# Kernel tuning notes

Measured on AMD Instinct MI355X. Metric: run time of the kernel, lower is better.

Reference implementation:

```python
import jax, jax.numpy as jnp
import numpy as np

N_GENE, N_TRAIN, N_EDGES = 20000, 4096, 131072
SRC, DST, H, OUT, NC = 2500, 2675, 2500, 2500, 16
EPS = 1e-5
SLOPE = 0.01  # torch default leaky_relu negative slope


def _leaky(x):
    return jnp.where(x >= 0, x, SLOPE * x)


def _bn(x, g, b):
    # BatchNorm1d, training-mode batch statistics over the node (batch) dim
    m = x.mean(axis=0)
    v = x.var(axis=0)
    return (x - m) * jax.lax.rsqrt(v + EPS) * g + b


def _ln(x, g, b):
    m = x.mean(axis=-1, keepdims=True)
    v = x.var(axis=-1, keepdims=True)
    return (x - m) * jax.lax.rsqrt(v + EPS) * g + b


def _sage(src_f, dst_f, si, di, W_self, W_neigh, b, n_dst):
    # DGL SAGEConv 'mean': fc_self(h_dst) + fc_neigh(mean over in-neighbors)
    msg = src_f[si]                                            # [E, d_src] gather
    agg = jax.ops.segment_sum(msg, di, num_segments=n_dst)     # [n_dst, d_src]
    deg = jax.ops.segment_sum(jnp.ones((si.shape[0],), src_f.dtype), di, num_segments=n_dst)
    mean = agg / jnp.maximum(deg, 1.0)[:, None]
    return dst_f @ W_self + mean @ W_neigh + b


def setup_inputs() -> dict:
    key = jax.random.key(0)
    ks = jax.random.split(key, 20)
    s = 0.02  # weight scale to keep deep 2500-dim chain numerically tame
    n = lambda k, shp: jax.random.normal(k, shp, dtype=jnp.float32)
    return {
        'gene_feats': n(ks[0], (N_GENE, SRC)),
        'train_feats': n(ks[1], (N_TRAIN, DST - NC)),
        'y_hat': n(ks[2], (N_TRAIN, NC)),
        'edge_src': jax.random.randint(ks[3], (N_EDGES,), 0, N_GENE, dtype=jnp.int32),
        'edge_dst': jax.random.randint(ks[4], (N_EDGES,), 0, N_TRAIN, dtype=jnp.int32),
        'W_self3': n(ks[5], (DST, H)) * s, 'W_neigh3': n(ks[6], (SRC, H)) * s, 'b3': jnp.zeros((H,), jnp.float32),
        'bn3_g': jnp.ones((H,), jnp.float32), 'bn3_b': jnp.zeros((H,), jnp.float32),
        'Wq': n(ks[7], (H, H)) * s, 'Wk': n(ks[8], (H, H)) * s, 'Wv': n(ks[9], (H, H)) * s,
        'bq': jnp.zeros((H,), jnp.float32), 'bk': jnp.zeros((H,), jnp.float32), 'bv': jnp.zeros((H,), jnp.float32),
        'Wo': n(ks[10], (H, H)) * s, 'bo': jnp.zeros((H,), jnp.float32),
        'ln2_g': jnp.ones((H,), jnp.float32), 'ln2_b': jnp.zeros((H,), jnp.float32),
        'W_self4': n(ks[11], (H, OUT)) * s, 'W_neigh4': n(ks[12], (SRC, OUT)) * s, 'b4': jnp.zeros((OUT,), jnp.float32),
        'bn4_g': jnp.ones((OUT,), jnp.float32), 'bn4_b': jnp.zeros((OUT,), jnp.float32),
        'W_lin2': n(ks[13], (OUT, OUT)) * s, 'b_lin2': jnp.zeros((OUT,), jnp.float32),
        'W_ce': n(ks[14], (OUT, NC)) * s, 'b_ce': jnp.zeros((NC,), jnp.float32),
    }


def reference(gene_feats, train_feats, y_hat, edge_src, edge_dst,
              W_self3, W_neigh3, b3, bn3_g, bn3_b,
              Wq, Wk, Wv, bq, bk, bv, Wo, bo, ln2_g, ln2_b,
              W_self4, W_neigh4, b4, bn4_g, bn4_b,
              W_lin2, b_lin2, W_ce, b_ce):
    # concat label logits onto train-node features (dst dim -> 2675)
    dst = jnp.concatenate([train_feats, y_hat], axis=1)
    # conv3: bipartite SAGE gene_node -> train_node
    h = _sage(gene_feats, dst, edge_src, edge_dst, W_self3, W_neigh3, b3, N_TRAIN)
    h = _leaky(_bn(h, bn3_g, bn3_b))
    # single-head self-attention over ALL train nodes as one sequence [L=N_TRAIN, E=H]
    q = h @ Wq + bq
    k = h @ Wk + bk
    v = h @ Wv + bv
    attn = jax.nn.softmax(q @ k.T * (1.0 / jnp.sqrt(jnp.asarray(H, h.dtype))), axis=-1)
    h = (attn @ v) @ Wo + bo
    h = _leaky(_ln(h, ln2_g, ln2_b))
    # (dropout omitted: eval-mode identity)
    # conv4: same graph, src = raw gene feats, dst = attention output
    h = _sage(gene_feats, h, edge_src, edge_dst, W_self4, W_neigh4, b4, N_TRAIN)
    x_hat = _leaky(_bn(h, bn4_g, bn4_b))
    y = jax.nn.relu(x_hat @ W_lin2 + b_lin2) @ W_ce + b_ce
    return (x_hat, y)
```

## Files before the change

kernel.cpp:

```cpp
#include <hip/hip_runtime.h>
#include <hip/hip_bf16.h>
#include <cstdint>
#include <cstddef>

constexpr int NTRAIN = 4096;
constexpr int NEDGES = 131072;
constexpr int DSRC = 2500, DH = 2500, DNC = 16;
constexpr int KD1 = 2659;
constexpr int KC3 = 5175;
constexpr int KP3 = 5184;
constexpr int KC4 = 5000;
constexpr int KP4 = 5056;
constexpr int KPH = 2560;
constexpr int NPW = 2560;
constexpr int GSTR = 2504;
constexpr float EPSV = 1e-5f;
constexpr float SLOPEV = 0.01f;

typedef __attribute__((ext_vector_type(8))) short bf16x8;
typedef __attribute__((ext_vector_type(4))) float f32x4;

static __device__ __forceinline__ unsigned short bfbits(float f) {
    __hip_bfloat16 h = __float2bfloat16(f);
    return *reinterpret_cast<unsigned short*>(&h);
}
static __device__ __forceinline__ float b2f(short s) {
    return __uint_as_float(((unsigned)(unsigned short)s) << 16);
}

__global__ void count_deg_k(const int* __restrict__ edst, int* __restrict__ deg) {
    int e = blockIdx.x * 256 + threadIdx.x;
    if (e < NEDGES) atomicAdd(&deg[edst[e]], 1);
}

__global__ __launch_bounds__(1024) void scan_deg_k(const int* __restrict__ deg,
                                                   int* __restrict__ indptr,
                                                   int* __restrict__ cursor) {
    __shared__ int sums[1024];
    int t = threadIdx.x;
    int base = t * 4;
    int d0 = deg[base + 0], d1 = deg[base + 1], d2 = deg[base + 2], d3 = deg[base + 3];
    sums[t] = d0 + d1 + d2 + d3;
    __syncthreads();
    for (int o = 1; o < 1024; o <<= 1) {
        int v = (t >= o) ? sums[t - o] : 0;
        __syncthreads();
        sums[t] += v;
        __syncthreads();
    }
    int excl = (t == 0) ? 0 : sums[t - 1];
    int p0 = excl, p1 = p0 + d0, p2 = p1 + d1, p3 = p2 + d2;
    indptr[base + 0] = p0; indptr[base + 1] = p1; indptr[base + 2] = p2; indptr[base + 3] = p3;
    cursor[base + 0] = p0; cursor[base + 1] = p1; cursor[base + 2] = p2; cursor[base + 3] = p3;
    if (t == 1023) indptr[4096] = p3 + d3;
}

__global__ void scatter_edges_k(const int* __restrict__ esrc, const int* __restrict__ edst,
                                int* __restrict__ cursor, int* __restrict__ csr_src) {
    int e = blockIdx.x * 256 + threadIdx.x;
    if (e < NEDGES) {
        int d = edst[e];
        int p = atomicAdd(&cursor[d], 1);
        csr_src[p] = esrc[e];
    }
}

__global__ __launch_bounds__(256) void gene2bf_k(const float* __restrict__ gene,
                                                 short* __restrict__ gbf) {
    int v = blockIdx.x * 256 + threadIdx.x;
    if (v >= 313) return;
    int row = blockIdx.y;
    const float* src = gene + (size_t)row * DSRC + v * 8;
    f32x4 a = *(const f32x4*)(src);
    f32x4 b = {0.f, 0.f, 0.f, 0.f};
    if (v < 312) b = *(const f32x4*)(src + 4);
    bf16x8 o;
#pragma unroll
    for (int c = 0; c < 4; c++) o[c] = (short)bfbits(a[c]);
#pragma unroll
    for (int c = 0; c < 4; c++) o[4 + c] = (short)bfbits(b[c]);
    *(bf16x8*)(gbf + (size_t)row * GSTR + v * 8) = o;
}

__global__ __launch_bounds__(256) void sage_mean_k(const short* __restrict__ gbf,
                                                   const int* __restrict__ indptr,
                                                   const int* __restrict__ csr_src,
                                                   __hip_bfloat16* __restrict__ A3,
                                                   __hip_bfloat16* __restrict__ A4) {
    int row = blockIdx.x;
    int s = indptr[row], e = indptr[row + 1];
    int t = threadIdx.x;
    float a0[8], a1[8];
#pragma unroll
    for (int c = 0; c < 8; c++) { a0[c] = 0.f; a1[c] = 0.f; }
    bool has1 = (t < 57);
    int j = s;
    for (; j + 2 <= e; j += 2) {
        const bf16x8* g0 = (const bf16x8*)(gbf + (size_t)csr_src[j] * GSTR);
        const bf16x8* g1 = (const bf16x8*)(gbf + (size_t)csr_src[j + 1] * GSTR);
        bf16x8 u0 = g0[t], w0 = g1[t];
        bf16x8 u1, w1;
        if (has1) { u1 = g0[t + 256]; w1 = g1[t + 256]; }
#pragma unroll
        for (int c = 0; c < 8; c++) a0[c] += b2f(u0[c]) + b2f(w0[c]);
        if (has1) {
#pragma unroll
            for (int c = 0; c < 8; c++) a1[c] += b2f(u1[c]) + b2f(w1[c]);
        }
    }
    if (j < e) {
        const bf16x8* g0 = (const bf16x8*)(gbf + (size_t)csr_src[j] * GSTR);
        bf16x8 u0 = g0[t];
#pragma unroll
        for (int c = 0; c < 8; c++) a0[c] += b2f(u0[c]);
        if (has1) {
            bf16x8 u1 = g0[t + 256];
#pragma unroll
            for (int c = 0; c < 8; c++) a1[c] += b2f(u1[c]);
        }
    }
    float inv = 1.f / fmaxf((float)(e - s), 1.f);
#pragma unroll
    for (int c = 0; c < 8; c++) {
        int f = t * 8 + c;
        __hip_bfloat16 h = __float2bfloat16(a0[c] * inv);
        A3[(size_t)row * KP3 + 2675 + f] = h;
        A4[(size_t)row * KP4 + 2500 + f] = h;
    }
    if (has1) {
#pragma unroll
        for (int c = 0; c < 8; c++) {
            int f = (t + 256) * 8 + c;
            if (f < 2500) {
                __hip_bfloat16 h = __float2bfloat16(a1[c] * inv);
                A3[(size_t)row * KP3 + 2675 + f] = h;
                A4[(size_t)row * KP4 + 2500 + f] = h;
            }
        }
    }
}

__global__ void dst_build_k(const float* __restrict__ trainf, const float* __restrict__ yhat,
                            __hip_bfloat16* __restrict__ A3) {
    int c = blockIdx.x * 256 + threadIdx.x;
    int r = blockIdx.y;
    if (c >= KP3) return;
    if (c >= 2675 && c < KC3) return;
    float v = 0.f;
    if (c < KD1) v = trainf[(size_t)r * KD1 + c];
    else if (c < 2675) v = yhat[r * DNC + (c - KD1)];
    A3[(size_t)r * KP3 + c] = __float2bfloat16(v);
}

__global__ __launch_bounds__(256) void wtrans_k(const float* __restrict__ W1,
                                                const float* __restrict__ W2, int ldw,
                                                __hip_bfloat16* __restrict__ Wt,
                                                int Nreal, int K1, int K12, int Kpad, int Npad) {
    __shared__ float tile[32][33];
    int k0 = blockIdx.x * 32, n0 = blockIdx.y * 32;
    int x = threadIdx.x & 31, y = threadIdx.x >> 5;
#pragma unroll
    for (int i = 0; i < 32; i += 8) {
        int k = k0 + y + i, n = n0 + x;
        float v = 0.f;
        if (n < Nreal) {
            if (k < K1) v = W1[(size_t)k * ldw + n];
            else if (k < K12) v = W2[(size_t)(k - K1) * ldw + n];
        }
        tile[y + i][x] = v;
    }
    __syncthreads();
#pragma unroll
    for (int i = 0; i < 32; i += 8) {
        int n = n0 + y + i, k = k0 + x;
        if (n < Npad && k < Kpad) Wt[(size_t)n * Kpad + k] = __float2bfloat16(tile[x][y + i]);
    }
}

__device__ __forceinline__ void async_cp16(const void* g, void* l) {
    __builtin_amdgcn_global_load_lds((const __attribute__((address_space(1))) void*)g,
                                     (__attribute__((address_space(3))) void*)l, 16, 0, 0);
}
#define WAITVM(N) asm volatile("s_waitcnt vmcnt(" #N ")" ::: "memory")
static __device__ __forceinline__ void bar_raw() {
    asm volatile("" ::: "memory");
    __builtin_amdgcn_s_barrier();
    asm volatile("" ::: "memory");
}

__global__ __launch_bounds__(512, 2) void gemm256_k(const short* __restrict__ A,
                                                    const short* __restrict__ Bt,
                                                    const float* __restrict__ bias,
                                                    float* __restrict__ Cf,
                                                    __hip_bfloat16* __restrict__ Cb,
                                                    int N, int K, int sA, int sB, int ldc,
                                                    float alpha, int act) {
    __shared__ short smem[65536];
    int nwg = gridDim.x * gridDim.y;
    int orig = blockIdx.y * gridDim.x + blockIdx.x;
    int qd = nwg >> 3, rr = nwg & 7;
    int xcd = orig & 7, oidx = orig >> 3;
    int nb = (xcd < rr ? xcd * (qd + 1) : rr * (qd + 1) + (xcd - rr) * qd) + oidx;
    int bx = nb % gridDim.x, by = nb / gridDim.x;
    int row0 = by * 256, col0 = bx * 256;

    int tid = threadIdx.x;
    int wave = tid >> 6, lane = tid & 63;
    int wm = wave >> 2, wn = wave & 3;

    int rsub = lane >> 2;
    int cs = ((lane & 3) * 8) ^ ((lane >= 32) ? 16 : 0);
    const short* gA0 = A + (size_t)(row0 + wave * 16 + rsub) * sA + cs;
    const short* gA1 = A + (size_t)(row0 + wave * 16 + 128 + rsub) * sA + cs;
    const short* gB0 = Bt + (size_t)(col0 + wave * 16 + rsub) * sB + cs;
    const short* gB1 = Bt + (size_t)(col0 + wave * 16 + 128 + rsub) * sB + cs;
    int sa0 = wave * 1024;
    int sa1 = (wave + 8) * 1024;

    int fr = lane & 15, kq = lane >> 4;
    int roff = fr * 32 + ((kq * 8) ^ ((fr & 8) ? 16 : 0));

    f32x4 acc[8][4];
#pragma unroll
    for (int i = 0; i < 8; i++)
#pragma unroll
        for (int j = 0; j < 4; j++)
#pragma unroll
            for (int r = 0; r < 4; r++) acc[i][j][r] = 0.f;

#define STAGE_A(kb, b, k0s) { \
    short* l0 = smem + (b) * 32768 + sa0 + (kb) * 512; \
    short* l1 = smem + (b) * 32768 + sa1 + (kb) * 512; \
    async_cp16(gA0 + (k0s) + (kb) * 32, l0); \
    async_cp16(gA1 + (k0s) + (kb) * 32, l1); }
#define STAGE_B(kb, b, k0s) { \
    short* l0 = smem + (b) * 32768 + 16384 + sa0 + (kb) * 512; \
    short* l1 = smem + (b) * 32768 + 16384 + sa1 + (kb) * 512; \
    async_cp16(gB0 + (k0s) + (kb) * 32, l0); \
    async_cp16(gB1 + (k0s) + (kb) * 32, l1); }
#define PHASE(b, kk, mq) { \
    const short* ab = smem + (b) * 32768; \
    const short* bb = smem + (b) * 32768 + 16384; \
    bf16x8 af[4], bv[4]; \
    _Pragma("unroll") for (int i = 0; i < 4; i++) \
        af[i] = *(const bf16x8*)(ab + (((wm * 8 + (mq) * 4 + i) * 2 + (kk)) << 9) + roff); \
    _Pragma("unroll") for (int j = 0; j < 4; j++) \
        bv[j] = *(const bf16x8*)(bb + (((wn * 4 + j) * 2 + (kk)) << 9) + roff); \
    __builtin_amdgcn_s_setprio(1); \
    _Pragma("unroll") for (int i = 0; i < 4; i++) \
        _Pragma("unroll") for (int j = 0; j < 4; j++) \
            acc[(mq) * 4 + i][j] = __builtin_amdgcn_mfma_f32_16x16x32_bf16(af[i], bv[j], acc[(mq) * 4 + i][j], 0, 0, 0); \
    __builtin_amdgcn_s_setprio(0); }

    int nt = K >> 6;
    STAGE_A(0, 0, 0); STAGE_B(0, 0, 0); STAGE_A(1, 0, 0); STAGE_B(1, 0, 0);
    int buf = 0;
    for (int t = 0; t < nt - 1; ++t) {
        int k1 = (t + 1) << 6;
        WAITVM(4); bar_raw();
        STAGE_A(0, buf ^ 1, k1);
        PHASE(buf, 0, 0);
        STAGE_B(0, buf ^ 1, k1);
        PHASE(buf, 0, 1);
        WAITVM(4); bar_raw();
        STAGE_A(1, buf ^ 1, k1);
        PHASE(buf, 1, 0);
        STAGE_B(1, buf ^ 1, k1);
        PHASE(buf, 1, 1);
        buf ^= 1;
    }
    WAITVM(4); bar_raw();
    PHASE(buf, 0, 0); PHASE(buf, 0, 1);
    WAITVM(0); bar_raw();
    PHASE(buf, 1, 0); PHASE(buf, 1, 1);
#undef STAGE_A
#undef STAGE_B
#undef PHASE

    int cn = lane & 15, cm = kq * 4;
    int mbase = row0 + wm * 128, nbase = col0 + wn * 64;
    if (Cb) {
#pragma unroll
        for (int j = 0; j < 4; j++) {
            int n = nbase + j * 16 + cn;
            if (n >= ldc) continue;
            bool real = n < N;
            float bvv = (real && bias) ? bias[n] : 0.f;
#pragma unroll
            for (int i = 0; i < 8; i++) {
#pragma unroll
                for (int r = 0; r < 4; r++) {
                    int m = mbase + i * 16 + cm + r;
                    float c = real ? alpha * acc[i][j][r] + bvv : 0.f;
                    if (act) c = fmaxf(c, 0.f);
                    Cb[(size_t)m * ldc + n] = __float2bfloat16(c);
                }
            }
        }
    } else {
#pragma unroll
        for (int j = 0; j < 4; j++) {
            int n = nbase + j * 16 + cn;
            if (n >= N) continue;
            float bvv = bias ? bias[n] : 0.f;
#pragma unroll
            for (int i = 0; i < 8; i++) {
#pragma unroll
                for (int r = 0; r < 4; r++) {
                    int m = mbase + i * 16 + cm + r;
                    float c = alpha * acc[i][j][r] + bvv;
                    if (act) c = fmaxf(c, 0.f);
                    Cf[(size_t)m * ldc + n] = c;
                }
            }
        }
    }
}

__global__ __launch_bounds__(256) void bn_partial_k(const float* __restrict__ X,
                                                    double* __restrict__ ps, double* __restrict__ ps2,
                                                    int M, int Ncol, int rowsPer) {
    int c = blockIdx.x * 256 + threadIdx.x;
    if (c >= Ncol) return;
    int r0 = blockIdx.y * rowsPer;
    int r1 = min(r0 + rowsPer, M);
    double s = 0, s2 = 0;
    for (int r = r0; r < r1; r++) {
        float x = X[(size_t)r * Ncol + c];
        s += x;
        s2 += (double)x * x;
    }
    ps[(size_t)blockIdx.y * Ncol + c] = s;
    ps2[(size_t)blockIdx.y * Ncol + c] = s2;
}

__global__ void bn_finalize_k(const double* __restrict__ ps, const double* __restrict__ ps2,
                              const float* __restrict__ g, const float* __restrict__ b,
                              float* __restrict__ scale, float* __restrict__ shift,
                              int Ncol, int nParts, int M) {
    int c = blockIdx.x * 256 + threadIdx.x;
    if (c >= Ncol) return;
    double s = 0, s2 = 0;
    for (int p = 0; p < nParts; p++) {
        s += ps[(size_t)p * Ncol + c];
        s2 += ps2[(size_t)p * Ncol + c];
    }
    double m = s / M;
    double v = s2 / M - m * m;
    float sc = g[c] / sqrtf((float)v + EPSV);
    scale[c] = sc;
    shift[c] = b[c] - (float)m * sc;
}

__global__ void bn_apply_k(const float* __restrict__ X, const float* __restrict__ scale,
                           const float* __restrict__ shift, __hip_bfloat16* __restrict__ Yb,
                           float* __restrict__ Yf, int Nreal, int Cpad) {
    int c = blockIdx.x * 256 + threadIdx.x;
    int r = blockIdx.y;
    if (c >= Cpad) return;
    float v = 0.f;
    if (c < Nreal) {
        v = fmaf(X[(size_t)r * Nreal + c], scale[c], shift[c]);
        v = v >= 0.f ? v : SLOPEV * v;
        if (Yf) Yf[(size_t)r * Nreal + c] = v;
    }
    Yb[(size_t)r * Cpad + c] = __float2bfloat16(v);
}

__device__ __forceinline__ double wave_sum_d(double v) {
#pragma unroll
    for (int o = 32; o > 0; o >>= 1) v += __shfl_down(v, o, 64);
    return v;
}
__device__ __forceinline__ float wave_sum_f(float v) {
#pragma unroll
    for (int o = 32; o > 0; o >>= 1) v += __shfl_down(v, o, 64);
    return v;
}
__device__ __forceinline__ float wave_max_f(float v) {
#pragma unroll
    for (int o = 32; o > 0; o >>= 1) v = fmaxf(v, __shfl_down(v, o, 64));
    return v;
}

__global__ __launch_bounds__(256) void ln_leaky_k(const float* __restrict__ X,
                                                  const float* __restrict__ g,
                                                  const float* __restrict__ b,
                                                  __hip_bfloat16* __restrict__ A4) {
    int row = blockIdx.x;
    const float* xr = X + (size_t)row * DH;
    double s = 0, s2 = 0;
    for (int c = threadIdx.x; c < DH; c += 256) {
        float x = xr[c];
        s += x;
        s2 += (double)x * x;
    }
    __shared__ double sb[4], sb2[4];
    int lane = threadIdx.x & 63, w = threadIdx.x >> 6;
    s = wave_sum_d(s);
    s2 = wave_sum_d(s2);
    if (lane == 0) { sb[w] = s; sb2[w] = s2; }
    __syncthreads();
    double S = sb[0] + sb[1] + sb[2] + sb[3];
    double S2 = sb2[0] + sb2[1] + sb2[2] + sb2[3];
    double m = S / DH;
    double v = S2 / DH - m * m;
    float inv = 1.f / sqrtf((float)v + EPSV);
    float mf = (float)m;
    __hip_bfloat16* yr = A4 + (size_t)row * KP4;
    for (int c = threadIdx.x; c < DH; c += 256) {
        float x = (xr[c] - mf) * inv * g[c] + b[c];
        x = x >= 0.f ? x : SLOPEV * x;
        yr[c] = __float2bfloat16(x);
    }
    if (threadIdx.x < KP4 - KC4) yr[KC4 + threadIdx.x] = __float2bfloat16(0.f);
}

__global__ __launch_bounds__(256) void softmax1_k(const float* __restrict__ X,
                                                  __hip_bfloat16* __restrict__ Y) {
    int row = blockIdx.x, t = threadIdx.x;
    const f32x4* xr = reinterpret_cast<const f32x4*>(X + (size_t)row * NTRAIN);
    f32x4 v[4];
    float mx = -3.4e38f;
#pragma unroll
    for (int i = 0; i < 4; i++) {
        v[i] = xr[i * 256 + t];
#pragma unroll
        for (int c = 0; c < 4; c++) mx = fmaxf(mx, v[i][c]);
    }
    __shared__ float sb[4];
    int lane = t & 63, w = t >> 6;
    mx = wave_max_f(mx);
    if (lane == 0) sb[w] = mx;
    __syncthreads();
    mx = fmaxf(fmaxf(sb[0], sb[1]), fmaxf(sb[2], sb[3]));
    float s = 0.f;
#pragma unroll
    for (int i = 0; i < 4; i++)
#pragma unroll
        for (int c = 0; c < 4; c++) {
            float e = expf(v[i][c] - mx);
            v[i][c] = e;
            s += e;
        }
    s = wave_sum_f(s);
    __syncthreads();
    if (lane == 0) sb[w] = s;
    __syncthreads();
    float inv = 1.f / (sb[0] + sb[1] + sb[2] + sb[3]);
    ushort4* yr = reinterpret_cast<ushort4*>(Y + (size_t)row * NTRAIN);
#pragma unroll
    for (int i = 0; i < 4; i++) {
        ushort4 o;
        o.x = bfbits(v[i][0] * inv);
        o.y = bfbits(v[i][1] * inv);
        o.z = bfbits(v[i][2] * inv);
        o.w = bfbits(v[i][3] * inv);
        yr[i * 256 + t] = o;
    }
}

__global__ __launch_bounds__(256) void head_k(const float* __restrict__ X,
                                              const float* __restrict__ Wce,
                                              const float* __restrict__ bce,
                                              float* __restrict__ Y) {
    int row = blockIdx.x;
    int n = threadIdx.x & 15, part = threadIdx.x >> 4;
    const float* xr = X + (size_t)row * DH;
    float s = 0.f;
    for (int k = part; k < DH; k += 16) s += xr[k] * Wce[k * 16 + n];
    __shared__ float red[256];
    red[threadIdx.x] = s;
    __syncthreads();
    for (int off = 8; off >= 1; off >>= 1) {
        if (part < off) red[threadIdx.x] += red[threadIdx.x + off * 16];
        __syncthreads();
    }
    if (part == 0) Y[row * 16 + n] = red[n] + bce[n];
}

extern "C" void kernel_launch(void* const* d_in, const int* in_sizes, int n_in,
                              void* d_out, int out_size, void* d_ws, size_t ws_size,
                              hipStream_t stream) {
    const float* gene    = (const float*)d_in[0];
    const float* trainf  = (const float*)d_in[1];
    const float* yhat    = (const float*)d_in[2];
    const int*   esrc    = (const int*)d_in[3];
    const int*   edst    = (const int*)d_in[4];
    const float* W_self3 = (const float*)d_in[5];
    const float* W_neigh3= (const float*)d_in[6];
    const float* b3      = (const float*)d_in[7];
    const float* bn3_g   = (const float*)d_in[8];
    const float* bn3_b   = (const float*)d_in[9];
    const float* Wq      = (const float*)d_in[10];
    const float* Wk      = (const float*)d_in[11];
    const float* Wv      = (const float*)d_in[12];
    const float* bq      = (const float*)d_in[13];
    const float* bk      = (const float*)d_in[14];
    const float* bv      = (const float*)d_in[15];
    const float* Wo      = (const float*)d_in[16];
    const float* bo      = (const float*)d_in[17];
    const float* ln2_g   = (const float*)d_in[18];
    const float* ln2_b   = (const float*)d_in[19];
    const float* W_self4 = (const float*)d_in[20];
    const float* W_neigh4= (const float*)d_in[21];
    const float* b4      = (const float*)d_in[22];
    const float* bn4_g   = (const float*)d_in[23];
    const float* bn4_b   = (const float*)d_in[24];
    const float* W_lin2  = (const float*)d_in[25];
    const float* b_lin2  = (const float*)d_in[26];
    const float* W_ce    = (const float*)d_in[27];
    const float* b_ce    = (const float*)d_in[28];

    char* ws = (char*)d_ws;
    size_t off = 0;
    auto alloc = [&](size_t bytes) -> void* {
        void* p = ws + off;
        off = (off + bytes + 255) & ~(size_t)255;
        return p;
    };
    __hip_bfloat16* A3cat  = (__hip_bfloat16*)alloc((size_t)NTRAIN * KP3 * 2);
    __hip_bfloat16* A4cat  = (__hip_bfloat16*)alloc((size_t)NTRAIN * KP4 * 2);
    __hip_bfloat16* h_bf   = (__hip_bfloat16*)alloc((size_t)NTRAIN * KPH * 2);
    __hip_bfloat16* q_bf   = (__hip_bfloat16*)alloc((size_t)NTRAIN * KPH * 2);
    __hip_bfloat16* k_bf   = (__hip_bfloat16*)alloc((size_t)NTRAIN * KPH * 2);
    __hip_bfloat16* vT_bf  = (__hip_bfloat16*)alloc((size_t)NPW * NTRAIN * 2);
    __hip_bfloat16* W3t    = (__hip_bfloat16*)alloc((size_t)NPW * KP3 * 2);
    __hip_bfloat16* Wqt    = (__hip_bfloat16*)alloc((size_t)NPW * KPH * 2);
    __hip_bfloat16* Wkt    = (__hip_bfloat16*)alloc((size_t)NPW * KPH * 2);
    __hip_bfloat16* Wvt    = (__hip_bfloat16*)alloc((size_t)NPW * KPH * 2);
    float*  bigC   = (float*)alloc((size_t)NTRAIN * NTRAIN * 4);
    double* ps     = (double*)alloc((size_t)16 * DH * 8);
    double* ps2    = (double*)alloc((size_t)16 * DH * 8);
    float*  scale  = (float*)alloc(DH * 4);
    float*  shift  = (float*)alloc(DH * 4);
    int*    deg    = (int*)alloc(NTRAIN * 4);
    int*    indptr = (int*)alloc((NTRAIN + 1) * 4);
    int*    cursor = (int*)alloc(NTRAIN * 4);
    int*    csr_src= (int*)alloc(NEDGES * 4);
    __hip_bfloat16* attn_bf = A3cat;
    __hip_bfloat16* W4t     = W3t;
    __hip_bfloat16* Wot     = Wkt;
    __hip_bfloat16* Wlin2t  = Wqt;
    __hip_bfloat16* xhat_bf = h_bf;
    __hip_bfloat16* ao_bf   = q_bf;
    short* gene_bf = (short*)W3t;

    float* xhat = (float*)d_out;
    float* yout = (float*)d_out + (size_t)NTRAIN * DH;

    auto gemm = [&](const void* A, const void* Bt, const float* bias, float* Cf,
                    __hip_bfloat16* Cb, int NpadCols, int Nreal, int K,
                    int sA, int sB, int ldc, float alpha, int act) {
        dim3 g(NpadCols / 256, NTRAIN / 256);
        gemm256_k<<<g, 512, 0, stream>>>((const short*)A, (const short*)Bt, bias, Cf, Cb,
                                         Nreal, K, sA, sB, ldc, alpha, act);
    };

    hipMemsetAsync(deg, 0, NTRAIN * 4, stream);
    count_deg_k<<<NEDGES / 256, 256, 0, stream>>>(edst, deg);
    scan_deg_k<<<1, 1024, 0, stream>>>(deg, indptr, cursor);
    scatter_edges_k<<<NEDGES / 256, 256, 0, stream>>>(esrc, edst, cursor, csr_src);
    gene2bf_k<<<dim3(2, 20000), 256, 0, stream>>>(gene, gene_bf);
    sage_mean_k<<<NTRAIN, 256, 0, stream>>>(gene_bf, indptr, csr_src, A3cat, A4cat);
    dst_build_k<<<dim3((KP3 + 255) / 256, NTRAIN), 256, 0, stream>>>(trainf, yhat, A3cat);
    wtrans_k<<<dim3(KP3 / 32, NPW / 32), 256, 0, stream>>>(W_self3, W_neigh3, DH, W3t, DH, 2675, KC3, KP3, NPW);

    gemm(A3cat, W3t, b3, bigC, nullptr, NPW, DH, KP3, KP3, KP3, DH, 1.f, 0);
    bn_partial_k<<<dim3((DH + 255) / 256, 16), 256, 0, stream>>>(bigC, ps, ps2, NTRAIN, DH, NTRAIN / 16);
    bn_finalize_k<<<(DH + 255) / 256, 256, 0, stream>>>(ps, ps2, bn3_g, bn3_b, scale, shift, DH, 16, NTRAIN);
    bn_apply_k<<<dim3((KPH + 255) / 256, NTRAIN), 256, 0, stream>>>(bigC, scale, shift, h_bf, nullptr, DH, KPH);

    wtrans_k<<<dim3(KPH / 32, NPW / 32), 256, 0, stream>>>(Wq, nullptr, DH, Wqt, DH, DH, DH, KPH, NPW);
    wtrans_k<<<dim3(KPH / 32, NPW / 32), 256, 0, stream>>>(Wk, nullptr, DH, Wkt, DH, DH, DH, KPH, NPW);
    wtrans_k<<<dim3(KPH / 32, NPW / 32), 256, 0, stream>>>(Wv, nullptr, DH, Wvt, DH, DH, DH, KPH, NPW);
    gemm(h_bf, Wqt, bq, nullptr, q_bf, NPW, DH, KPH, KPH, KPH, KPH, 1.f, 0);
    gemm(h_bf, Wkt, bk, nullptr, k_bf, NPW, DH, KPH, KPH, KPH, KPH, 1.f, 0);
    gemm(h_bf, Wvt, bv, bigC, nullptr, NPW, DH, KPH, KPH, KPH, DH, 1.f, 0);
    wtrans_k<<<dim3(NTRAIN / 32, NPW / 32), 256, 0, stream>>>(bigC, nullptr, DH, vT_bf, DH, NTRAIN, NTRAIN, NTRAIN, NPW);
    gemm(q_bf, k_bf, nullptr, bigC, nullptr, NTRAIN, NTRAIN, KPH, KPH, KPH, NTRAIN, 0.02f, 0);
    softmax1_k<<<NTRAIN, 256, 0, stream>>>(bigC, attn_bf);
    gemm(attn_bf, vT_bf, nullptr, nullptr, ao_bf, NPW, DH, NTRAIN, NTRAIN, NTRAIN, KPH, 1.f, 0);
    wtrans_k<<<dim3(KPH / 32, NPW / 32), 256, 0, stream>>>(Wo, nullptr, DH, Wot, DH, DH, DH, KPH, NPW);
    gemm(ao_bf, Wot, bo, bigC, nullptr, NPW, DH, KPH, KPH, KPH, DH, 1.f, 0);
    ln_leaky_k<<<NTRAIN, 256, 0, stream>>>(bigC, ln2_g, ln2_b, A4cat);

    wtrans_k<<<dim3(KP4 / 32, NPW / 32), 256, 0, stream>>>(W_self4, W_neigh4, DH, W4t, DH, DH, KC4, KP4, NPW);
    gemm(A4cat, W4t, b4, bigC, nullptr, NPW, DH, KP4, KP4, KP4, DH, 1.f, 0);
    bn_partial_k<<<dim3((DH + 255) / 256, 16), 256, 0, stream>>>(bigC, ps, ps2, NTRAIN, DH, NTRAIN / 16);
    bn_finalize_k<<<(DH + 255) / 256, 256, 0, stream>>>(ps, ps2, bn4_g, bn4_b, scale, shift, DH, 16, NTRAIN);
    bn_apply_k<<<dim3((KPH + 255) / 256, NTRAIN), 256, 0, stream>>>(bigC, scale, shift, xhat_bf, xhat, DH, KPH);

    wtrans_k<<<dim3(KPH / 32, NPW / 32), 256, 0, stream>>>(W_lin2, nullptr, DH, Wlin2t, DH, DH, DH, KPH, NPW);
    gemm(xhat_bf, Wlin2t, b_lin2, bigC, nullptr, NPW, DH, KPH, KPH, KPH, DH, 1.f, 1);
    head_k<<<NTRAIN, 256, 0, stream>>>(bigC, W_ce, b_ce, yout);
    (void)ws_size; (void)n_in; (void)in_sizes; (void)out_size;
}
```

Before: 1.828 ms.

## Fuse QKV projections into one GEMM and restructure GEMM LDS/MFMA pipeline

Concatenates the transposed Wq/Wk/Wv weights into one 7680-column B matrix with a combined bias, so Q, K and V come out of a single GEMM as bf16. V is transposed straight from bf16, which drops the fp32 V round trip through bigC. The GEMM main loop is also reworked to issue LDS fragment reads ahead of the MFMA blocks, with explicit barriers, lgkmcnt waits and sched_barriers around each MFMA group. This trades fewer launches and less memory traffic for more barriers per k-step, and adds a modulo test in the bf16 epilogue to zero the padded columns of each section.

```diff
diff --git a/kernel.cpp b/kernel.cpp
--- a/kernel.cpp
+++ b/kernel.cpp
@@ -13,6 +13,7 @@
 constexpr int KP4 = 5056;
 constexpr int KPH = 2560;
 constexpr int NPW = 2560;
+constexpr int NQKV = 7680;
 constexpr int GSTR = 2504;
 constexpr float EPSV = 1e-5f;
 constexpr float SLOPEV = 0.01f;
@@ -177,11 +178,36 @@
     }
 }
 
+__global__ __launch_bounds__(256) void btrans_k(const __hip_bfloat16* __restrict__ V, int ldv,
+                                                __hip_bfloat16* __restrict__ VT) {
+    __shared__ __hip_bfloat16 tile[32][33];
+    int r0 = blockIdx.x * 32, c0 = blockIdx.y * 32;
+    int x = threadIdx.x & 31, y = threadIdx.x >> 5;
+#pragma unroll
+    for (int i = 0; i < 32; i += 8)
+        tile[y + i][x] = V[(size_t)(r0 + y + i) * ldv + c0 + x];
+    __syncthreads();
+#pragma unroll
+    for (int i = 0; i < 32; i += 8)
+        VT[(size_t)(c0 + y + i) * NTRAIN + r0 + x] = tile[x][y + i];
+}
+
+__global__ void qkv_bias_k(const float* __restrict__ bq, const float* __restrict__ bk,
+                           const float* __restrict__ bv, float* __restrict__ bqkv) {
+    int i = blockIdx.x * 256 + threadIdx.x;
+    if (i >= NQKV) return;
+    int j = i / KPH, c = i % KPH;
+    const float* src = (j == 0) ? bq : (j == 1) ? bk : bv;
+    bqkv[i] = (c < DH) ? src[c] : 0.f;
+}
+
 __device__ __forceinline__ void async_cp16(const void* g, void* l) {
     __builtin_amdgcn_global_load_lds((const __attribute__((address_space(1))) void*)g,
                                      (__attribute__((address_space(3))) void*)l, 16, 0, 0);
 }
 #define WAITVM(N) asm volatile("s_waitcnt vmcnt(" #N ")" ::: "memory")
+#define LGKM0 asm volatile("s_waitcnt lgkmcnt(0)" ::: "memory")
+#define SB __builtin_amdgcn_sched_barrier(0)
 static __device__ __forceinline__ void bar_raw() {
     asm volatile("" ::: "memory");
     __builtin_amdgcn_s_barrier();
@@ -194,7 +220,7 @@
                                                     float* __restrict__ Cf,
                                                     __hip_bfloat16* __restrict__ Cb,
                                                     int N, int K, int sA, int sB, int ldc,
-                                                    float alpha, int act) {
+                                                    int nmod, float alpha, int act) {
     __shared__ short smem[65536];
     int nwg = gridDim.x * gridDim.y;
     int orig = blockIdx.y * gridDim.x + blockIdx.x;
@@ -238,44 +264,80 @@
     short* l1 = smem + (b) * 32768 + 16384 + sa1 + (kb) * 512; \
     async_cp16(gB0 + (k0s) + (kb) * 32, l0); \
     async_cp16(gB1 + (k0s) + (kb) * 32, l1); }
-#define PHASE(b, kk, mq) { \
-    const short* ab = smem + (b) * 32768; \
-    const short* bb = smem + (b) * 32768 + 16384; \
-    bf16x8 af[4], bv[4]; \
+#define DSRA(dst, mq, kk) \
     _Pragma("unroll") for (int i = 0; i < 4; i++) \
-        af[i] = *(const bf16x8*)(ab + (((wm * 8 + (mq) * 4 + i) * 2 + (kk)) << 9) + roff); \
+        dst[i] = *(const bf16x8*)(ab + (((wm * 8 + (mq) * 4 + i) * 2 + (kk)) << 9) + roff);
+#define DSRB(dst, kk) \
     _Pragma("unroll") for (int j = 0; j < 4; j++) \
-        bv[j] = *(const bf16x8*)(bb + (((wn * 4 + j) * 2 + (kk)) << 9) + roff); \
+        dst[j] = *(const bf16x8*)(bb + (((wn * 4 + j) * 2 + (kk)) << 9) + roff);
+#define MFMA16(av, bvv, mq) \
     __builtin_amdgcn_s_setprio(1); \
     _Pragma("unroll") for (int i = 0; i < 4; i++) \
         _Pragma("unroll") for (int j = 0; j < 4; j++) \
-            acc[(mq) * 4 + i][j] = __builtin_amdgcn_mfma_f32_16x16x32_bf16(af[i], bv[j], acc[(mq) * 4 + i][j], 0, 0, 0); \
-    __builtin_amdgcn_s_setprio(0); }
+            acc[(mq) * 4 + i][j] = __builtin_amdgcn_mfma_f32_16x16x32_bf16(av[i], bvv[j], acc[(mq) * 4 + i][j], 0, 0, 0); \
+    __builtin_amdgcn_s_setprio(0);
 
     int nt = K >> 6;
     STAGE_A(0, 0, 0); STAGE_B(0, 0, 0); STAGE_A(1, 0, 0); STAGE_B(1, 0, 0);
+    WAITVM(4);
+    bar_raw();
     int buf = 0;
     for (int t = 0; t < nt - 1; ++t) {
+        const short* ab = smem + (buf << 15);
+        const short* bb = ab + 16384;
         int k1 = (t + 1) << 6;
-        WAITVM(4); bar_raw();
+        bf16x8 a0[4], a1[4], b0[4], b1[4];
+        DSRA(a0, 0, 0); DSRB(b0, 0);
         STAGE_A(0, buf ^ 1, k1);
-        PHASE(buf, 0, 0);
+        bar_raw(); LGKM0; SB;
+        MFMA16(a0, b0, 0);
+        SB; bar_raw();
+        DSRA(a1, 1, 0);
         STAGE_B(0, buf ^ 1, k1);
-        PHASE(buf, 0, 1);
-        WAITVM(4); bar_raw();
+        WAITVM(4);
+        bar_raw(); LGKM0; SB;
+        MFMA16(a1, b0, 1);
+        SB; bar_raw();
+        DSRA(a0, 0, 1); DSRB(b1, 1);
         STAGE_A(1, buf ^ 1, k1);
-        PHASE(buf, 1, 0);
+        bar_raw(); LGKM0; SB;
+        MFMA16(a0, b1, 0);
+        SB; bar_raw();
+        DSRA(a1, 1, 1);
         STAGE_B(1, buf ^ 1, k1);
-        PHASE(buf, 1, 1);
+        WAITVM(4);
+        bar_raw(); LGKM0; SB;
+        MFMA16(a1, b1, 1);
+        SB; bar_raw();
         buf ^= 1;
     }
-    WAITVM(4); bar_raw();
-    PHASE(buf, 0, 0); PHASE(buf, 0, 1);
-    WAITVM(0); bar_raw();
-    PHASE(buf, 1, 0); PHASE(buf, 1, 1);
+    {
+        const short* ab = smem + (buf << 15);
+        const short* bb = ab + 16384;
+        bf16x8 a0[4], a1[4], b0[4], b1[4];
+        DSRA(a0, 0, 0); DSRB(b0, 0);
+        bar_raw(); LGKM0; SB;
+        MFMA16(a0, b0, 0);
+        SB; bar_raw();
+        DSRA(a1, 1, 0);
+        WAITVM(0);
+        bar_raw(); LGKM0; SB;
+        MFMA16(a1, b0, 1);
+        SB; bar_raw();
+        DSRA(a0, 0, 1); DSRB(b1, 1);
+        bar_raw(); LGKM0; SB;
+        MFMA16(a0, b1, 0);
+        SB; bar_raw();
+        DSRA(a1, 1, 1);
+        bar_raw(); LGKM0; SB;
+        MFMA16(a1, b1, 1);
+        SB;
+    }
 #undef STAGE_A
 #undef STAGE_B
-#undef PHASE
+#undef DSRA
+#undef DSRB
+#undef MFMA16
 
     int cn = lane & 15, cm = kq * 4;
     int mbase = row0 + wm * 128, nbase = col0 + wn * 64;
@@ -284,7 +346,7 @@
         for (int j = 0; j < 4; j++) {
             int n = nbase + j * 16 + cn;
             if (n >= ldc) continue;
-            bool real = n < N;
+            bool real = (n % nmod) < N;
             float bvv = (real && bias) ? bias[n] : 0.f;
 #pragma unroll
             for (int i = 0; i < 8; i++) {
@@ -522,28 +584,26 @@
     __hip_bfloat16* A3cat  = (__hip_bfloat16*)alloc((size_t)NTRAIN * KP3 * 2);
     __hip_bfloat16* A4cat  = (__hip_bfloat16*)alloc((size_t)NTRAIN * KP4 * 2);
     __hip_bfloat16* h_bf   = (__hip_bfloat16*)alloc((size_t)NTRAIN * KPH * 2);
-    __hip_bfloat16* q_bf   = (__hip_bfloat16*)alloc((size_t)NTRAIN * KPH * 2);
-    __hip_bfloat16* k_bf   = (__hip_bfloat16*)alloc((size_t)NTRAIN * KPH * 2);
-    __hip_bfloat16* vT_bf  = (__hip_bfloat16*)alloc((size_t)NPW * NTRAIN * 2);
+    __hip_bfloat16* qkv_bf = (__hip_bfloat16*)alloc((size_t)NTRAIN * NQKV * 2);
     __hip_bfloat16* W3t    = (__hip_bfloat16*)alloc((size_t)NPW * KP3 * 2);
-    __hip_bfloat16* Wqt    = (__hip_bfloat16*)alloc((size_t)NPW * KPH * 2);
-    __hip_bfloat16* Wkt    = (__hip_bfloat16*)alloc((size_t)NPW * KPH * 2);
-    __hip_bfloat16* Wvt    = (__hip_bfloat16*)alloc((size_t)NPW * KPH * 2);
+    __hip_bfloat16* Wqkvt  = (__hip_bfloat16*)alloc((size_t)3 * NPW * KPH * 2);
     float*  bigC   = (float*)alloc((size_t)NTRAIN * NTRAIN * 4);
     double* ps     = (double*)alloc((size_t)16 * DH * 8);
     double* ps2    = (double*)alloc((size_t)16 * DH * 8);
     float*  scale  = (float*)alloc(DH * 4);
     float*  shift  = (float*)alloc(DH * 4);
+    float*  bqkv   = (float*)alloc(NQKV * 4);
     int*    deg    = (int*)alloc(NTRAIN * 4);
     int*    indptr = (int*)alloc((NTRAIN + 1) * 4);
     int*    cursor = (int*)alloc(NTRAIN * 4);
     int*    csr_src= (int*)alloc(NEDGES * 4);
     __hip_bfloat16* attn_bf = A3cat;
     __hip_bfloat16* W4t     = W3t;
-    __hip_bfloat16* Wot     = Wkt;
-    __hip_bfloat16* Wlin2t  = Wqt;
+    __hip_bfloat16* Wot     = Wqkvt;
+    __hip_bfloat16* Wlin2t  = Wqkvt;
     __hip_bfloat16* xhat_bf = h_bf;
-    __hip_bfloat16* ao_bf   = q_bf;
+    __hip_bfloat16* ao_bf   = qkv_bf;
+    __hip_bfloat16* vT_bf   = (__hip_bfloat16*)bigC;
     short* gene_bf = (short*)W3t;
 
     float* xhat = (float*)d_out;
@@ -551,10 +611,10 @@
 
     auto gemm = [&](const void* A, const void* Bt, const float* bias, float* Cf,
                     __hip_bfloat16* Cb, int NpadCols, int Nreal, int K,
-                    int sA, int sB, int ldc, float alpha, int act) {
+                    int sA, int sB, int ldc, int nmod, float alpha, int act) {
         dim3 g(NpadCols / 256, NTRAIN / 256);
         gemm256_k<<<g, 512, 0, stream>>>((const short*)A, (const short*)Bt, bias, Cf, Cb,
-                                         Nreal, K, sA, sB, ldc, alpha, act);
+                                         Nreal, K, sA, sB, ldc, nmod, alpha, act);
     };
 
     hipMemsetAsync(deg, 0, NTRAIN * 4, stream);
@@ -566,33 +626,32 @@
     dst_build_k<<<dim3((KP3 + 255) / 256, NTRAIN), 256, 0, stream>>>(trainf, yhat, A3cat);
     wtrans_k<<<dim3(KP3 / 32, NPW / 32), 256, 0, stream>>>(W_self3, W_neigh3, DH, W3t, DH, 2675, KC3, KP3, NPW);
 
-    gemm(A3cat, W3t, b3, bigC, nullptr, NPW, DH, KP3, KP3, KP3, DH, 1.f, 0);
+    gemm(A3cat, W3t, b3, bigC, nullptr, NPW, DH, KP3, KP3, KP3, DH, DH, 1.f, 0);
     bn_partial_k<<<dim3((DH + 255) / 256, 16), 256, 0, stream>>>(bigC, ps, ps2, NTRAIN, DH, NTRAIN / 16);
     bn_finalize_k<<<(DH + 255) / 256, 256, 0, stream>>>(ps, ps2, bn3_g, bn3_b, scale, shift, DH, 16, NTRAIN);
     bn_apply_k<<<dim3((KPH + 255) / 256, NTRAIN), 256, 0, stream>>>(bigC, scale, shift, h_bf, nullptr, DH, KPH);
 
-    wtrans_k<<<dim3(KPH / 32, NPW / 32), 256, 0, stream>>>(Wq, nullptr, DH, Wqt, DH, DH, DH, KPH, NPW);
-    wtrans_k<<<dim3(KPH / 32, NPW / 32), 256, 0, stream>>>(Wk, nullptr, DH, Wkt, DH, DH, DH, KPH, NPW);
-    wtrans_k<<<dim3(KPH / 32, NPW / 32), 256, 0, stream>>>(Wv, nullptr, DH, Wvt, DH, DH, DH, KPH, NPW);
-    gemm(h_bf, Wqt, bq, nullptr, q_bf, NPW, DH, KPH, KPH, KPH, KPH, 1.f, 0);
-    gemm(h_bf, Wkt, bk, nullptr, k_bf, NPW, DH, KPH, KPH, KPH, KPH, 1.f, 0);
-    gemm(h_bf, Wvt, bv, bigC, nullptr, NPW, DH, KPH, KPH, KPH, DH, 1.f, 0);
-    wtrans_k<<<dim3(NTRAIN / 32, NPW / 32), 256, 0, stream>>>(bigC, nullptr, DH, vT_bf, DH, NTRAIN, NTRAIN, NTRAIN, NPW);
-    gemm(q_bf, k_bf, nullptr, bigC, nullptr, NTRAIN, NTRAIN, KPH, KPH, KPH, NTRAIN, 0.02f, 0);
+    wtrans_k<<<dim3(KPH / 32, NPW / 32), 256, 0, stream>>>(Wq, nullptr, DH, Wqkvt, DH, DH, DH, KPH, NPW);
+    wtrans_k<<<dim3(KPH / 32, NPW / 32), 256, 0, stream>>>(Wk, nullptr, DH, Wqkvt + (size_t)NPW * KPH, DH, DH, DH, KPH, NPW);
+    wtrans_k<<<dim3(KPH / 32, NPW / 32), 256, 0, stream>>>(Wv, nullptr, DH, Wqkvt + (size_t)2 * NPW * KPH, DH, DH, DH, KPH, NPW);
+    qkv_bias_k<<<NQKV / 256, 256, 0, stream>>>(bq, bk, bv, bqkv);
+    gemm(h_bf, Wqkvt, bqkv, nullptr, qkv_bf, NQKV, DH, KPH, KPH, KPH, NQKV, KPH, 1.f, 0);
+    gemm(qkv_bf, qkv_bf + KPH, nullptr, bigC, nullptr, NTRAIN, NTRAIN, KPH, NQKV, NQKV, NTRAIN, NTRAIN, 0.02f, 0);
     softmax1_k<<<NTRAIN, 256, 0, stream>>>(bigC, attn_bf);
-    gemm(attn_bf, vT_bf, nullptr, nullptr, ao_bf, NPW, DH, NTRAIN, NTRAIN, NTRAIN, KPH, 1.f, 0);
+    btrans_k<<<dim3(NTRAIN / 32, KPH / 32), 256, 0, stream>>>(qkv_bf + 2 * KPH, NQKV, vT_bf);
+    gemm(attn_bf, vT_bf, nullptr, nullptr, ao_bf, NPW, DH, NTRAIN, NTRAIN, NTRAIN, KPH, KPH, 1.f, 0);
     wtrans_k<<<dim3(KPH / 32, NPW / 32), 256, 0, stream>>>(Wo, nullptr, DH, Wot, DH, DH, DH, KPH, NPW);
-    gemm(ao_bf, Wot, bo, bigC, nullptr, NPW, DH, KPH, KPH, KPH, DH, 1.f, 0);
+    gemm(ao_bf, Wot, bo, bigC, nullptr, NPW, DH, KPH, KPH, KPH, DH, DH, 1.f, 0);
     ln_leaky_k<<<NTRAIN, 256, 0, stream>>>(bigC, ln2_g, ln2_b, A4cat);
 
     wtrans_k<<<dim3(KP4 / 32, NPW / 32), 256, 0, stream>>>(W_self4, W_neigh4, DH, W4t, DH, DH, KC4, KP4, NPW);
-    gemm(A4cat, W4t, b4, bigC, nullptr, NPW, DH, KP4, KP4, KP4, DH, 1.f, 0);
+    gemm(A4cat, W4t, b4, bigC, nullptr, NPW, DH, KP4, KP4, KP4, DH, DH, 1.f, 0);
     bn_partial_k<<<dim3((DH + 255) / 256, 16), 256, 0, stream>>>(bigC, ps, ps2, NTRAIN, DH, NTRAIN / 16);
     bn_finalize_k<<<(DH + 255) / 256, 256, 0, stream>>>(ps, ps2, bn4_g, bn4_b, scale, shift, DH, 16, NTRAIN);
     bn_apply_k<<<dim3((KPH + 255) / 256, NTRAIN), 256, 0, stream>>>(bigC, scale, shift, xhat_bf, xhat, DH, KPH);
 
     wtrans_k<<<dim3(KPH / 32, NPW / 32), 256, 0, stream>>>(W_lin2, nullptr, DH, Wlin2t, DH, DH, DH, KPH, NPW);
-    gemm(xhat_bf, Wlin2t, b_lin2, bigC, nullptr, NPW, DH, KPH, KPH, KPH, DH, 1.f, 1);
+    gemm(xhat_bf, Wlin2t, b_lin2, bigC, nullptr, NPW, DH, KPH, KPH, KPH, DH, DH, 1.f, 1);
     head_k<<<NTRAIN, 256, 0, stream>>>(bigC, W_ce, b_ce, yout);
     (void)ws_size; (void)n_in; (void)in_sizes; (void)out_size;
 }
```

Measured after the change: 1.796 ms (median of 2 runs). About the same (-1.7%).
